# Optimization experiments

Measured on AMD Instinct MI355X. Metric: run time of the kernel, lower is better.

Reference implementation:

```python
import jax, jax.numpy as jnp
import numpy as np

THRESH = 0.5      # jaccard_thresh
NEGPOS = 3        # neg:pos ratio for hard negative mining
VAR0, VAR1 = 0.1, 0.2  # SSD encoding variances


def point_form(boxes):
    # center-size [P,4] -> (xmin,ymin,xmax,ymax)
    return jnp.concatenate([boxes[:, :2] - boxes[:, 2:] / 2,
                            boxes[:, :2] + boxes[:, 2:] / 2], axis=1)


def jaccard(box_a, box_b):
    # box_a [O,4], box_b [P,4] point-form -> IoU [O,P]
    lt = jnp.maximum(box_a[:, None, :2], box_b[None, :, :2])
    rb = jnp.minimum(box_a[:, None, 2:], box_b[None, :, 2:])
    wh = jnp.clip(rb - lt, 0.0)
    inter = wh[..., 0] * wh[..., 1]
    area_a = ((box_a[:, 2] - box_a[:, 0]) * (box_a[:, 3] - box_a[:, 1]))[:, None]
    area_b = ((box_b[:, 2] - box_b[:, 0]) * (box_b[:, 3] - box_b[:, 1]))[None, :]
    return inter / (area_a + area_b - inter)


def encode(matched, priors):
    # matched point-form [P,4], priors center-size [P,4]
    g_cxcy = ((matched[:, :2] + matched[:, 2:]) / 2 - priors[:, :2]) / (VAR0 * priors[:, 2:])
    g_wh = jnp.log((matched[:, 2:] - matched[:, :2]) / priors[:, 2:]) / VAR1
    return jnp.concatenate([g_cxcy, g_wh], axis=1)


def match_one(truths, labels, priors):
    # truths [O,4] point-form, labels [O] int, priors [P,4] center-size
    O = truths.shape[0]
    ov = jaccard(truths, point_form(priors))          # [O,P]
    best_prior_idx = jnp.argmax(ov, axis=1)           # [O]
    best_truth_ov = jnp.max(ov, axis=0)               # [P]
    best_truth_idx = jnp.argmax(ov, axis=0)           # [P]
    # ensure each gt matches its best prior
    best_truth_ov = best_truth_ov.at[best_prior_idx].set(2.0)
    best_truth_idx = best_truth_idx.at[best_prior_idx].set(jnp.arange(O))
    matches = truths[best_truth_idx]                  # [P,4]
    conf = jnp.where(best_truth_ov < THRESH, 0, labels[best_truth_idx] + 1)
    return encode(matches, priors), conf


def setup_inputs() -> dict:
    key = jax.random.key(0)
    ks = jax.random.split(key, 6)
    B, P, C, O = 32, 24656, 81, 16
    predictions = jax.random.normal(ks[0], (B, P, 4 + C), dtype=jnp.float32)
    # priors: center-size, valid w/h
    pc = jax.random.uniform(ks[1], (P, 2), minval=0.05, maxval=0.95)
    pwh = jax.random.uniform(ks[2], (P, 2), minval=0.02, maxval=0.3)
    priors = jnp.concatenate([pc, pwh], axis=1).astype(jnp.float32)
    # ground-truth boxes in point form, guaranteed positive extent
    tc = jax.random.uniform(ks[3], (B, O, 2), minval=0.2, maxval=0.8)
    twh = jax.random.uniform(ks[4], (B, O, 2), minval=0.05, maxval=0.3)
    targets_boxes = jnp.concatenate([tc - twh / 2, tc + twh / 2], axis=-1).astype(jnp.float32)
    targets_labels = jax.random.randint(ks[5], (B, O), 0, C - 1, dtype=jnp.int32)
    return {"predictions": predictions, "targets_boxes": targets_boxes,
            "targets_labels": targets_labels, "priors": priors}


def reference(predictions, targets_boxes, targets_labels, priors):
    loc_data = predictions[..., :4]        # [B,P,4]
    conf_data = predictions[..., 4:]       # [B,P,C]
    B, P = loc_data.shape[:2]
    C = conf_data.shape[2]

    loc_t, conf_t = jax.vmap(match_one, in_axes=(0, 0, None))(
        targets_boxes, targets_labels, priors)   # [B,P,4], [B,P]

    pos = conf_t > 0                                   # [B,P]
    # smooth L1 on positives, sum reduction
    d = loc_data - loc_t
    ad = jnp.abs(d)
    sl1 = jnp.where(ad < 1.0, 0.5 * d * d, ad - 0.5)
    loss_l = jnp.sum(sl1 * pos[..., None].astype(sl1.dtype))

    # per-anchor cross entropy
    logp = jax.nn.log_softmax(conf_data, axis=-1)
    lbl = jnp.clip(conf_t, 0, C - 1)
    ce = -jnp.take_along_axis(logp, lbl[..., None], axis=-1)[..., 0]  # [B,P]

    # hard negative mining: rank negatives by loss (positives zeroed)
    loss_rank = jnp.where(pos, 0.0, ce)
    loss_idx = jnp.argsort(-loss_rank, axis=1)
    idx_rank = jnp.argsort(loss_idx, axis=1)
    num_pos = jnp.sum(pos, axis=1, keepdims=True)          # [B,1]
    num_neg = jnp.minimum(num_pos * NEGPOS, P)
    neg = idx_rank < num_neg

    sel = (pos | neg).astype(ce.dtype)
    loss_c = jnp.sum(ce * sel)

    N = jnp.sum(num_pos).astype(loss_l.dtype)
    return loss_l / N, loss_c / N
```

## Files before the change

### kernel.cpp

```cpp
#include <hip/hip_runtime.h>
#include <math.h>

#define NB 32
#define NP 24656
#define NO 16
#define NC 81
#define ND 85
#define THRESH_F 0.5f
#define NEGPOS_I 3
#define VAR0_F 0.1f
#define VAR1_F 0.2f
#define NEG_HUGE -1e30f

#define BPCNT (NB * NP)
#define MBLK2 25
#define CHB32 771
#define SPB2 56
#define CB32 11264

typedef unsigned long long u64;

__global__ __launch_bounds__(256) void k_match(
    const float* __restrict__ tboxes, const float* __restrict__ priors,
    float2* __restrict__ bt2, u64* __restrict__ mcand,
    int* __restrict__ npos, float* __restrict__ accB, int* __restrict__ done) {
    const int b = blockIdx.y, bx = blockIdx.x, tid = threadIdx.x;
    __shared__ float tb[NO * 4];
    __shared__ u64 kbuf[NO][256];
    __shared__ u64 pbuf[NO][16];
    if (bx == 0 && b == 0) {
        if (tid < NB) npos[tid] = 0;
        if (tid < 2 * NB) accB[tid] = 0.f;
        if (tid == 0) *done = 0;
    }
    if (tid < NO * 4) tb[tid] = tboxes[b * NO * 4 + tid];
    __syncthreads();

    const int p0 = bx * 1024 + tid * 4;
    float pl[4], pt[4], prr[4], pbm[4], pa[4];
    bool pv[4];
#pragma unroll
    for (int j = 0; j < 4; ++j) {
        const int p = p0 + j;
        pv[j] = (p < NP);
        const float4 q = pv[j] ? ((const float4*)priors)[p]
                               : make_float4(0.f, 0.f, 1.f, 1.f);
        pl[j] = q.x - q.z * 0.5f; pt[j] = q.y - q.w * 0.5f;
        prr[j] = q.x + q.z * 0.5f; pbm[j] = q.y + q.w * 0.5f;
        pa[j] = (prr[j] - pl[j]) * (pbm[j] - pt[j]);
    }
    float bestv[4] = {-1.f, -1.f, -1.f, -1.f};
    int besti[4] = {0, 0, 0, 0};
    for (int o = 0; o < NO; ++o) {
        const float al = tb[o * 4], at = tb[o * 4 + 1];
        const float ar = tb[o * 4 + 2], ab = tb[o * 4 + 3];
        const float aarea = (ar - al) * (ab - at);
        u64 kmax = 0ull;
#pragma unroll
        for (int j = 0; j < 4; ++j) {
            float iw = fminf(ar, prr[j]) - fmaxf(al, pl[j]); iw = fmaxf(iw, 0.f);
            float ih = fminf(ab, pbm[j]) - fmaxf(at, pt[j]); ih = fmaxf(ih, 0.f);
            const float inter = iw * ih;
            const float iou = inter / (aarea + pa[j] - inter);
            if (pv[j]) {
                if (iou > bestv[j]) { bestv[j] = iou; besti[j] = o; }
                const u64 key = ((u64)__float_as_uint(iou) << 32) |
                                (u64)(0xFFFFFFFFu - (unsigned)(p0 + j));
                kmax = (key > kmax) ? key : kmax;
            }
        }
        kbuf[o][tid] = kmax;
    }
#pragma unroll
    for (int j = 0; j < 4; ++j)
        if (pv[j])
            bt2[(size_t)b * NP + p0 + j] =
                make_float2(bestv[j], __int_as_float(besti[j]));
    __syncthreads();
    {
        const int o = tid >> 4, seg = tid & 15;
        u64 m = kbuf[o][seg];
#pragma unroll
        for (int i = 1; i < 16; ++i) {
            const u64 v = kbuf[o][i * 16 + seg];
            m = (v > m) ? v : m;
        }
        pbuf[o][seg] = m;
    }
    __syncthreads();
    if (tid < NO) {
        u64 m = pbuf[tid][0];
#pragma unroll
        for (int i = 1; i < 16; ++i) {
            const u64 v = pbuf[tid][i];
            m = (v > m) ? v : m;
        }
        mcand[((size_t)(b * NO + tid)) * MBLK2 + bx] = m;
    }
}

__device__ __forceinline__ void stage_load(float4* vreg,
                                           const char* __restrict__ gpred,
                                           int b, int r0, int lane) {
    const size_t off = ((size_t)b * NP + r0) * 340ull;
    const char* g = gpred + off;
    const bool unsafe = (b == NB - 1) && (r0 + 34 > NP);
    if (!unsafe) {
#pragma unroll
        for (int k = 0; k < 11; ++k)
            vreg[k] = *(const float4*)(g + k * 1024 + lane * 16);
    } else {
        const int nf4 = (NP - r0) * ND / 4;
        const float4* gs = (const float4*)g;
#pragma unroll
        for (int k = 0; k < 11; ++k) {
            const int idx = k * 64 + lane;
            vreg[k] = (idx < nf4) ? gs[idx]
                                  : make_float4(0.f, 0.f, 0.f, 0.f);
        }
    }
}

__device__ __forceinline__ void stage_write(char* buf, const float4* vreg,
                                            int lane) {
#pragma unroll
    for (int k = 0; k < 11; ++k)
        *(float4*)(buf + k * 1024 + lane * 16) = vreg[k];
}

__global__ __launch_bounds__(64) void k_main(
    const float* __restrict__ pred, const float* __restrict__ tboxes,
    const int* __restrict__ tlabels, const float* __restrict__ priors,
    const float2* __restrict__ bt2, const u64* __restrict__ mcand,
    float* __restrict__ lr, int* __restrict__ npos, float* __restrict__ accB) {
    __shared__ char smem[2][CB32];

    const int b = blockIdx.y;
    const int span = blockIdx.x;
    const int lane = threadIdx.x;
    const size_t bbase = (size_t)b * NP;
    const char* gpred = (const char*)pred;

    char* cur = smem[0];
    char* nxt = smem[1];

    const int rho = lane >> 1;
    const int h = lane & 1;
    const int c0 = rho & 3;
    const int Ab = 16 * (21 * rho + (rho >> 2));
    const int sbase = h ? 11 : 1;

    u64 pbk = 0ull;
    if (lane < NO) {
        const u64* c = mcand + (size_t)(b * NO + lane) * MBLK2;
        for (int i = 0; i < MBLK2; ++i) {
            const u64 v = c[i];
            pbk = (v > pbk) ? v : pbk;
        }
    }
    int p16[NO];
#pragma unroll
    for (int j = 0; j < NO; ++j) {
        const u64 kj = __shfl(pbk, j, 64);
        p16[j] = (int)(0xFFFFFFFFu - (unsigned)(kj & 0xFFFFFFFFull));
    }

    float my_ll = 0.f, my_ce = 0.f;
    int my_np = 0;

    int chunk = span;
    int next_chunk = chunk + SPB2;
    {
        float4 vreg[11];
        stage_load(vreg, gpred, b, chunk * 32, lane);
        stage_write(cur, vreg, lane);
    }

    while (chunk < CHB32) {
        float4 vreg[11];
        const bool have_next = (next_chunk < CHB32);
        if (have_next)
            stage_load(vreg, gpred, b, next_chunk * 32, lane);

        const int r0 = chunk * 32;
        const int nrows = min(32, NP - r0);

        float4 v[11];
#pragma unroll
        for (int k = 0; k < 11; ++k)
            v[k] = *(const float4*)(cur + Ab + 16 * (sbase + k));

        float vals[44];
#pragma unroll
        for (int k = 0; k < 11; ++k) {
            const float xs[4] = {v[k].x, v[k].y, v[k].z, v[k].w};
#pragma unroll
            for (int t = 0; t < 4; ++t) {
                bool ok;
                if (k == 0)
                    ok = h ? false : (t >= c0);
                else if (k == 10)
                    ok = h ? (t <= c0) : true;
                else
                    ok = true;
                vals[4 * k + t] = ok ? xs[t] : NEG_HUGE;
            }
        }
        float mA = vals[0], mB = vals[1];
#pragma unroll
        for (int j = 2; j < 44; j += 2) {
            mA = fmaxf(mA, vals[j]);
            mB = fmaxf(mB, vals[j + 1]);
        }
        float m = fmaxf(mA, mB);
        m = fmaxf(m, __shfl_xor(m, 1, 64));

        float sA = 0.f, sB = 0.f;
#pragma unroll
        for (int j = 0; j < 44; j += 2) {
            sA += __expf(vals[j] - m);
            sB += __expf(vals[j + 1] - m);
        }
        float ssum = sA + sB;
        ssum += __shfl_xor(ssum, 1, 64);
        const float lse = m + __logf(ssum);

        if (h == 0 && rho < nrows) {
            const float bg = (c0 == 0) ? v[0].x : (c0 == 1) ? v[0].y
                           : (c0 == 2) ? v[0].z : v[0].w;
            const int p = r0 + rho;
            const float2 bt = bt2[bbase + p];
            int o_f = -1;
#pragma unroll
            for (int j = 0; j < NO; ++j)
                if (p == p16[j]) o_f = j;
            const bool forced = (o_f >= 0);
            const bool pos = forced || (bt.x >= THRESH_F);
            const int o = forced ? o_f : __float_as_int(bt.y);
            lr[bbase + p] = pos ? 0.f : (lse - bg);
            if (pos) {
                my_np += 1;
                const float* rowp = (const float*)(cur + 340 * rho);
                const int lbl = tlabels[b * NO + o] + 1;
                my_ce += lse - rowp[4 + lbl];
                const float4 pq = *((const float4*)priors + p);
                const float tx0 = tboxes[(b * NO + o) * 4 + 0];
                const float ty0 = tboxes[(b * NO + o) * 4 + 1];
                const float tx1 = tboxes[(b * NO + o) * 4 + 2];
                const float ty1 = tboxes[(b * NO + o) * 4 + 3];
                const float g0 = ((tx0 + tx1) * 0.5f - pq.x) / (VAR0_F * pq.z);
                const float g1 = ((ty0 + ty1) * 0.5f - pq.y) / (VAR0_F * pq.w);
                const float g2 = __logf((tx1 - tx0) / pq.z) / VAR1_F;
                const float g3 = __logf((ty1 - ty0) / pq.w) / VAR1_F;
                float dd, ad;
                dd = rowp[0] - g0; ad = fabsf(dd); my_ll += (ad < 1.f) ? 0.5f * dd * dd : (ad - 0.5f);
                dd = rowp[1] - g1; ad = fabsf(dd); my_ll += (ad < 1.f) ? 0.5f * dd * dd : (ad - 0.5f);
                dd = rowp[2] - g2; ad = fabsf(dd); my_ll += (ad < 1.f) ? 0.5f * dd * dd : (ad - 0.5f);
                dd = rowp[3] - g3; ad = fabsf(dd); my_ll += (ad < 1.f) ? 0.5f * dd * dd : (ad - 0.5f);
            }
        }

        if (have_next)
            stage_write(nxt, vreg, lane);

        chunk = next_chunk;
        next_chunk += SPB2;
        char* tmp = cur; cur = nxt; nxt = tmp;
    }

    for (int d2 = 1; d2 < 64; d2 <<= 1) {
        my_ll += __shfl_xor(my_ll, d2, 64);
        my_ce += __shfl_xor(my_ce, d2, 64);
        my_np += __shfl_xor(my_np, d2, 64);
    }
    if (lane == 0) {
        if (my_ll != 0.f) atomicAdd(&accB[b * 2 + 0], my_ll);
        if (my_ce != 0.f) atomicAdd(&accB[b * 2 + 1], my_ce);
        if (my_np) atomicAdd(&npos[b], my_np);
    }
}

__global__ __launch_bounds__(1024) void k_select(
    const float* __restrict__ lrk, const int* __restrict__ npos,
    float* __restrict__ accB, int* __restrict__ done, float* __restrict__ out) {
    const int b = blockIdx.x;
    const float4* row4 = (const float4*)(lrk + (size_t)b * NP);
    const int tid = threadIdx.x;
    const int lane = tid & 63;
    const int wid = tid >> 6;
    const int sub = lane & 15;

    __shared__ unsigned hist16[2048][16];
    __shared__ unsigned chist[2048];
    __shared__ int sh_bucket, sh_knew;
    __shared__ float wsum[16];
    __shared__ int wcnt[16];

    float4 cch[7];
    bool cvz[7];
#pragma unroll
    for (int j = 0; j < 7; ++j) {
        const int i = tid + j * 1024;
        cvz[j] = (i < NP / 4);
        cch[j] = cvz[j] ? row4[i] : make_float4(0.f, 0.f, 0.f, 0.f);
    }

    const int K0 = min(npos[b] * NEGPOS_I, NP);
    int k = K0;
    unsigned prefix = 0;

    const int shifts[3] = {21, 10, 0};
    const unsigned masks[3] = {0u, 0xFFE00000u, 0xFFFFFC00u};

    for (int pass = 0; pass < 3; ++pass) {
        const int shift = shifts[pass];
        const unsigned mask_hi = masks[pass];
        {
            uint4* hz = (uint4*)hist16;
            for (int j = tid; j < 2048 * 4; j += 1024)
                hz[j] = make_uint4(0u, 0u, 0u, 0u);
        }
        __syncthreads();
#pragma unroll
        for (int j = 0; j < 7; ++j) {
            if (cvz[j]) {
                const float4 v4 = cch[j];
#pragma unroll
                for (int c = 0; c < 4; ++c) {
                    const float f = (c == 0) ? v4.x : (c == 1) ? v4.y
                                  : (c == 2) ? v4.z : v4.w;
                    const unsigned v = __float_as_uint(f);
                    if ((v & mask_hi) == (prefix & mask_hi))
                        atomicAdd(&hist16[(v >> shift) & 2047u][sub], 1u);
                }
            }
        }
        __syncthreads();
        for (int j = tid; j < 2048; j += 1024) {
            const uint4* hp = (const uint4*)&hist16[j][0];
            const uint4 a = hp[0], b4 = hp[1], c4 = hp[2], d4 = hp[3];
            chist[j] = a.x + a.y + a.z + a.w + b4.x + b4.y + b4.z + b4.w +
                       c4.x + c4.y + c4.z + c4.w + d4.x + d4.y + d4.z + d4.w;
        }
        __syncthreads();
        if (tid < 64) {
            unsigned g = 0;
            for (int j = 0; j < 32; ++j) g += chist[lane * 32 + j];
            unsigned T = g;
            for (int d = 1; d < 64; d <<= 1) {
                const unsigned t = __shfl_down(T, d, 64);
                if (lane + d < 64) T += t;
            }
            const unsigned E = T - g;
            const bool hit = (E < (unsigned)k) && ((unsigned)k <= T);
            const unsigned long long msk = __ballot(hit);
            const int wl = __ffsll(msk) - 1;
            if (lane == wl) {
                unsigned cum = E;
                int bsel = lane * 32, kn = k;
                for (int j = 31; j >= 0; --j) {
                    const unsigned c = chist[lane * 32 + j];
                    if (cum + c >= (unsigned)k) {
                        bsel = lane * 32 + j;
                        kn = k - (int)cum;
                        break;
                    }
                    cum += c;
                }
                sh_bucket = bsel;
                sh_knew = kn;
            }
        }
        __syncthreads();
        prefix |= ((unsigned)sh_bucket) << shift;
        k = sh_knew;
        __syncthreads();
    }
    const float T = __uint_as_float(prefix);

    float msum = 0.f;
    int mcnt = 0;
#pragma unroll
    for (int j = 0; j < 7; ++j) {
        if (cvz[j]) {
            const float4 v4 = cch[j];
#pragma unroll
            for (int c = 0; c < 4; ++c) {
                const float f = (c == 0) ? v4.x : (c == 1) ? v4.y
                              : (c == 2) ? v4.z : v4.w;
                if (__float_as_uint(f) > prefix) { msum += f; mcnt++; }
            }
        }
    }
    for (int s = 32; s > 0; s >>= 1) {
        msum += __shfl_down(msum, s, 64);
        mcnt += __shfl_down(mcnt, s, 64);
    }
    if (lane == 0) { wsum[wid] = msum; wcnt[wid] = mcnt; }
    __syncthreads();
    if (tid == 0) {
        float tot = 0.f;
        int cnt = 0;
        for (int w = 0; w < 16; ++w) { tot += wsum[w]; cnt += wcnt[w]; }
        atomicAdd(&accB[b * 2 + 1], tot + (float)(K0 - cnt) * T);
        __threadfence();
        if (atomicAdd(done, 1) == NB - 1) {
            volatile const float* va = accB;
            volatile const int* vn = npos;
            int n = 0;
            float a0 = 0.f, a1 = 0.f;
            for (int bb = 0; bb < NB; ++bb) {
                n += vn[bb];
                a0 += va[bb * 2 + 0];
                a1 += va[bb * 2 + 1];
            }
            const float N = (float)n;
            out[0] = a0 / N;
            out[1] = a1 / N;
        }
    }
}

extern "C" void kernel_launch(void* const* d_in, const int* in_sizes, int n_in,
                              void* d_out, int out_size, void* d_ws, size_t ws_size,
                              hipStream_t stream) {
    const float* pred   = (const float*)d_in[0];
    const float* tboxes = (const float*)d_in[1];
    const int*   tlabels = (const int*)d_in[2];
    const float* priors = (const float*)d_in[3];
    float* out = (float*)d_out;

    char* w = (char*)d_ws;
    float2* bt2 = (float2*)w;
    float*  lrk = (float*)(w + 8ull * BPCNT);
    u64*    mcand = (u64*)(w + 12ull * BPCNT);
    char*   w2 = w + 12ull * BPCNT + 8ull * NB * NO * MBLK2;
    int*    npos = (int*)w2;
    float*  accB = (float*)(w2 + 4ull * NB);
    int*    done = (int*)(w2 + 4ull * NB + 8ull * NB);

    k_match<<<dim3(MBLK2, NB), dim3(256), 0, stream>>>(
        tboxes, priors, bt2, mcand, npos, accB, done);
    k_main<<<dim3(SPB2, NB), dim3(64), 0, stream>>>(
        pred, tboxes, tlabels, priors, bt2, mcand, lrk, npos, accB);
    k_select<<<dim3(NB), dim3(1024), 0, stream>>>(lrk, npos, accB, done, out);
}
```

Measured before the change: 107.8 us.

## Recompute per-prior best truth in main kernel instead of storing bt2

```diff
diff --git a/kernel.cpp b/kernel.cpp
--- a/kernel.cpp
+++ b/kernel.cpp
@@ -22,7 +22,7 @@
 
 __global__ __launch_bounds__(256) void k_match(
     const float* __restrict__ tboxes, const float* __restrict__ priors,
-    float2* __restrict__ bt2, u64* __restrict__ mcand,
+    u64* __restrict__ mcand,
     int* __restrict__ npos, float* __restrict__ accB, int* __restrict__ done) {
     const int b = blockIdx.y, bx = blockIdx.x, tid = threadIdx.x;
     __shared__ float tb[NO * 4];
@@ -49,8 +49,6 @@
         prr[j] = q.x + q.z * 0.5f; pbm[j] = q.y + q.w * 0.5f;
         pa[j] = (prr[j] - pl[j]) * (pbm[j] - pt[j]);
     }
-    float bestv[4] = {-1.f, -1.f, -1.f, -1.f};
-    int besti[4] = {0, 0, 0, 0};
     for (int o = 0; o < NO; ++o) {
         const float al = tb[o * 4], at = tb[o * 4 + 1];
         const float ar = tb[o * 4 + 2], ab = tb[o * 4 + 3];
@@ -63,7 +61,6 @@
             const float inter = iw * ih;
             const float iou = inter / (aarea + pa[j] - inter);
             if (pv[j]) {
-                if (iou > bestv[j]) { bestv[j] = iou; besti[j] = o; }
                 const u64 key = ((u64)__float_as_uint(iou) << 32) |
                                 (u64)(0xFFFFFFFFu - (unsigned)(p0 + j));
                 kmax = (key > kmax) ? key : kmax;
@@ -71,11 +68,6 @@
         }
         kbuf[o][tid] = kmax;
     }
-#pragma unroll
-    for (int j = 0; j < 4; ++j)
-        if (pv[j])
-            bt2[(size_t)b * NP + p0 + j] =
-                make_float2(bestv[j], __int_as_float(besti[j]));
     __syncthreads();
     {
         const int o = tid >> 4, seg = tid & 15;
@@ -131,9 +123,10 @@
 __global__ __launch_bounds__(64) void k_main(
     const float* __restrict__ pred, const float* __restrict__ tboxes,
     const int* __restrict__ tlabels, const float* __restrict__ priors,
-    const float2* __restrict__ bt2, const u64* __restrict__ mcand,
+    const u64* __restrict__ mcand,
     float* __restrict__ lr, int* __restrict__ npos, float* __restrict__ accB) {
     __shared__ char smem[2][CB32];
+    __shared__ float tbs[NO * 4];
 
     const int b = blockIdx.y;
     const int span = blockIdx.x;
@@ -149,6 +142,8 @@
     const int c0 = rho & 3;
     const int Ab = 16 * (21 * rho + (rho >> 2));
     const int sbase = h ? 11 : 1;
+
+    tbs[lane] = tboxes[b * NO * 4 + lane];
 
     u64 pbk = 0ull;
     if (lane < NO) {
@@ -184,6 +179,8 @@
 
         const int r0 = chunk * 32;
         const int nrows = min(32, NP - r0);
+        const int p = r0 + rho;
+        const bool rok = (rho < nrows);
 
         float4 v[11];
 #pragma unroll
@@ -225,18 +222,42 @@
         ssum += __shfl_xor(ssum, 1, 64);
         const float lse = m + __logf(ssum);
 
-        if (h == 0 && rho < nrows) {
+        float bv = -1.f;
+        int bi = 0;
+        {
+            const float4 pq = rok ? *((const float4*)priors + p)
+                                  : make_float4(0.f, 0.f, 1.f, 1.f);
+            const float prl = pq.x - pq.z * 0.5f, prt = pq.y - pq.w * 0.5f;
+            const float prr2 = pq.x + pq.z * 0.5f, prb = pq.y + pq.w * 0.5f;
+            const float parea = (prr2 - prl) * (prb - prt);
+            const int obase = h * 8;
+#pragma unroll
+            for (int oj = 0; oj < 8; ++oj) {
+                const int o = obase + oj;
+                const float al = tbs[o * 4 + 0], at = tbs[o * 4 + 1];
+                const float ar = tbs[o * 4 + 2], ab = tbs[o * 4 + 3];
+                float iw = fminf(ar, prr2) - fmaxf(al, prl); iw = fmaxf(iw, 0.f);
+                float ih = fminf(ab, prb) - fmaxf(at, prt); ih = fmaxf(ih, 0.f);
+                const float inter = iw * ih;
+                const float aarea = (ar - al) * (ab - at);
+                const float iou = inter / (aarea + parea - inter);
+                if (iou > bv) { bv = iou; bi = o; }
+            }
+            const float ov = __shfl_xor(bv, 1, 64);
+            const int oi = __shfl_xor(bi, 1, 64);
+            if (ov > bv || (ov == bv && oi < bi)) { bv = ov; bi = oi; }
+        }
+
+        if (h == 0 && rok) {
             const float bg = (c0 == 0) ? v[0].x : (c0 == 1) ? v[0].y
                            : (c0 == 2) ? v[0].z : v[0].w;
-            const int p = r0 + rho;
-            const float2 bt = bt2[bbase + p];
             int o_f = -1;
 #pragma unroll
             for (int j = 0; j < NO; ++j)
                 if (p == p16[j]) o_f = j;
             const bool forced = (o_f >= 0);
-            const bool pos = forced || (bt.x >= THRESH_F);
-            const int o = forced ? o_f : __float_as_int(bt.y);
+            const bool pos = forced || (bv >= THRESH_F);
+            const int o = forced ? o_f : bi;
             lr[bbase + p] = pos ? 0.f : (lse - bg);
             if (pos) {
                 my_np += 1;
@@ -244,10 +265,10 @@
                 const int lbl = tlabels[b * NO + o] + 1;
                 my_ce += lse - rowp[4 + lbl];
                 const float4 pq = *((const float4*)priors + p);
-                const float tx0 = tboxes[(b * NO + o) * 4 + 0];
-                const float ty0 = tboxes[(b * NO + o) * 4 + 1];
-                const float tx1 = tboxes[(b * NO + o) * 4 + 2];
-                const float ty1 = tboxes[(b * NO + o) * 4 + 3];
+                const float tx0 = tbs[o * 4 + 0];
+                const float ty0 = tbs[o * 4 + 1];
+                const float tx1 = tbs[o * 4 + 2];
+                const float ty1 = tbs[o * 4 + 3];
                 const float g0 = ((tx0 + tx1) * 0.5f - pq.x) / (VAR0_F * pq.z);
                 const float g1 = ((ty0 + ty1) * 0.5f - pq.y) / (VAR0_F * pq.w);
                 const float g2 = __logf((tx1 - tx0) / pq.z) / VAR1_F;
@@ -431,7 +452,6 @@
     float* out = (float*)d_out;
 
     char* w = (char*)d_ws;
-    float2* bt2 = (float2*)w;
     float*  lrk = (float*)(w + 8ull * BPCNT);
     u64*    mcand = (u64*)(w + 12ull * BPCNT);
     char*   w2 = w + 12ull * BPCNT + 8ull * NB * NO * MBLK2;
@@ -440,8 +460,8 @@
     int*    done = (int*)(w2 + 4ull * NB + 8ull * NB);
 
     k_match<<<dim3(MBLK2, NB), dim3(256), 0, stream>>>(
-        tboxes, priors, bt2, mcand, npos, accB, done);
+        tboxes, priors, mcand, npos, accB, done);
     k_main<<<dim3(SPB2, NB), dim3(64), 0, stream>>>(
-        pred, tboxes, tlabels, priors, bt2, mcand, lrk, npos, accB);
+        pred, tboxes, tlabels, priors, mcand, lrk, npos, accB);
     k_select<<<dim3(NB), dim3(1024), 0, stream>>>(lrk, npos, accB, done, out);
 }
```

New measurement: 108.2 us. No clear change (+0.3%).
